# Optimization experiments

Hardware: AMD Instinct MI355X
Metric: run time of the kernel (lower is better)

Reference implementation:

```python
import jax, jax.numpy as jnp
import numpy as np
import math

NUM_BANDS = 16
BINS = 1024
CROPSIZE = 1024
BATCH = 4


def setup_inputs() -> dict:
    key = jax.random.key(0)
    ks = jax.random.split(key, 10)
    s = 1.0 / math.sqrt(BINS)
    return {
        "x": jax.random.normal(ks[0], (BATCH, CROPSIZE, BINS), jnp.float32),
        "Wq": jax.random.normal(ks[1], (BINS, BINS), jnp.float32) * s,
        "bq": jax.random.normal(ks[2], (BINS,), jnp.float32) * 0.02,
        "Wk": jax.random.normal(ks[3], (BINS, BINS), jnp.float32) * s,
        "bk": jax.random.normal(ks[4], (BINS,), jnp.float32) * 0.02,
        "Wv": jax.random.normal(ks[5], (BINS, BINS), jnp.float32) * s,
        "bv": jax.random.normal(ks[6], (BINS,), jnp.float32) * 0.02,
        "Wo": jax.random.normal(ks[7], (BINS, BINS), jnp.float32) * s,
        "bo": jax.random.normal(ks[8], (BINS,), jnp.float32) * 0.02,
        "er": jax.random.normal(ks[9], (BINS // NUM_BANDS, CROPSIZE), jnp.float32),
    }


def reference(x, Wq, bq, Wk, bk, Wv, bv, Wo, bo, er):
    b, w, c = x.shape
    h = NUM_BANDS
    d = c // h
    # Linear projections (torch Linear: x @ W.T + b)
    q = (jnp.einsum("bwc,oc->bwo", x, Wq) + bq).reshape(b, w, h, d).transpose(0, 2, 1, 3)  # [b,h,w,d]
    k = (jnp.einsum("bwc,oc->bwo", x, Wk) + bk).reshape(b, w, h, d).transpose(0, 2, 1, 3)  # [b,h,w,d]
    v = (jnp.einsum("bwc,oc->bwo", x, Wv) + bv).reshape(b, w, h, d).transpose(0, 2, 1, 3)  # [b,h,w,d]
    # relative-position bias via skew trick
    qe = jnp.einsum("bhwd,dc->bhwc", q, er)  # [b,h,w,cropsize]
    qe = jnp.pad(qe, ((0, 0), (0, 0), (0, 0), (1, 0)))  # pad last dim on left -> [b,h,w,crop+1]
    p = jnp.swapaxes(qe, 2, 3)[:, :, 1:, :]  # [b,h,crop,w] == [b,h,w,w] since crop==w
    qk = (jnp.einsum("bhwd,bhud->bhwu", q, k) + p) / math.sqrt(c)
    a = jax.nn.softmax(qk, axis=-1)
    av = jnp.einsum("bhwu,bhud->bhwd", a, v).transpose(0, 2, 1, 3).reshape(b, w, c)
    return jnp.einsum("bwc,oc->bwo", av, Wo) + bo
```

## Files before the change

### kernel.cpp

```cpp
#include <hip/hip_runtime.h>
#include <stdint.h>

typedef __attribute__((ext_vector_type(8))) short   short8;
typedef __attribute__((ext_vector_type(8))) __bf16  bf16x8;
typedef __attribute__((ext_vector_type(4))) float   floatx4;

__device__ __forceinline__ float bf2f(uint16_t h) {
    union { uint32_t u; float f; } v; v.u = ((uint32_t)h) << 16; return v.f;
}
__device__ __forceinline__ uint16_t f2bf(float f) {
    union { float f; uint32_t u; } v; v.f = f;
    uint32_t u = v.u;
    u += 0x7FFFu + ((u >> 16) & 1u);
    return (uint16_t)(u >> 16);
}
__device__ __forceinline__ floatx4 mfma16(short8 a, short8 b, floatx4 c) {
    return __builtin_amdgcn_mfma_f32_16x16x32_bf16(
        __builtin_bit_cast(bf16x8, a), __builtin_bit_cast(bf16x8, b), c, 0, 0, 0);
}
__device__ __forceinline__ void gll16(const short* g, short* l) {
    __builtin_amdgcn_global_load_lds(
        (const __attribute__((address_space(1))) uint32_t*)g,
        (__attribute__((address_space(3))) uint32_t*)l, 16, 0, 0);
}

__global__ void conv_all(
    const float* __restrict__ x,
    const float* __restrict__ Wq, const float* __restrict__ Wk,
    const float* __restrict__ Wv, const float* __restrict__ Wo,
    const float* __restrict__ bq, const float* __restrict__ bk,
    const float* __restrict__ bv, const float* __restrict__ bo,
    const float* __restrict__ er,
    short* __restrict__ xb, short* __restrict__ Wb,
    short* __restrict__ ball, short* __restrict__ ErT)
{
    int blk = blockIdx.x, tid = threadIdx.x;
    if (blk < 4096) {
        int i = blk * 256 + tid;
        float4 v = ((const float4*)x)[i];
        ((short4*)xb)[i] = make_short4((short)f2bf(v.x), (short)f2bf(v.y),
                                       (short)f2bf(v.z), (short)f2bf(v.w));
    } else if (blk < 8192) {
        int rel = blk - 4096;
        int wsel = rel >> 10;
        int i = (rel & 1023) * 256 + tid;
        const float* W = (wsel == 0) ? Wq : (wsel == 1) ? Wk : (wsel == 2) ? Wv : Wo;
        float4 v = ((const float4*)W)[i];
        ((short4*)(Wb + ((size_t)wsel << 20)))[i] =
            make_short4((short)f2bf(v.x), (short)f2bf(v.y),
                        (short)f2bf(v.z), (short)f2bf(v.w));
    } else if (blk < 8448) {
        int idx = (blk - 8192) * 256 + tid;
        int w = idx >> 6, d = idx & 63;
        ErT[idx] = (short)f2bf(er[d * 1024 + w]);
    } else {
        int idx = (blk - 8448) * 256 + tid;
        int sel = idx >> 10, j = idx & 1023;
        const float* s = (sel == 0) ? bq : (sel == 1) ? bk : (sel == 2) ? bv : bo;
        ball[idx] = (short)f2bf(s[j]);
    }
}

#define VM0  asm volatile("s_waitcnt vmcnt(0)" ::: "memory")
#define BARR asm volatile("s_barrier" ::: "memory")

__device__ __forceinline__ void stage_unit(const short* src, short* region, int tid)
{
    const int row  = tid >> 3;
    const int scol = (((tid & 7) ^ (row & 7)) << 3);
    gll16(src + (size_t)row * 1024 + scol, region + tid * 8);
}

#define SAU(buf, u) (As + (buf) * 16384 + (u) * 4096)
#define SBU(buf, u) (Bs + (buf) * 12288 + (u) * 4096)
#define STG_A(buf, u, kt) stage_unit(Asrc + (size_t)(u) * 65536 + (size_t)(kt) * 64, SAU(buf, u), tid)
#define STG_B(buf, u, kt) stage_unit(Bsrc + (size_t)(u) * 65536 + (size_t)(kt) * 64, SBU(buf, u), tid)
#define STG7(buf, kt) do { \
    STG_A(buf, 0, kt); STG_A(buf, 1, kt); STG_A(buf, 2, kt); STG_A(buf, 3, kt); \
    STG_B(buf, 0, kt); STG_B(buf, 1, kt); STG_B(buf, 2, kt); } while (0)

#define RD_A(buf) do { \
    _Pragma("unroll") for (int fr_ = 0; fr_ < 8; ++fr_) { \
        const short* p_ = SAU(buf, wm * 2 + (fr_ >> 2)) + ((fr_ & 3) * 16 + lrow) * 64; \
        _Pragma("unroll") for (int ks_ = 0; ks_ < 2; ++ks_) \
            a[fr_][ks_] = *(const short8*)&p_[((ks_ * 4 + quad) ^ rx) << 3]; \
    } } while (0)

#define RD_B(buf, c) do { \
    const short* p_ = SBU(buf, c) + (wn * 16 + lrow) * 64; \
    _Pragma("unroll") for (int ks_ = 0; ks_ < 2; ++ks_) \
        bb[ks_] = *(const short8*)&p_[((ks_ * 4 + quad) ^ rx) << 3]; \
    } while (0)

#define MFMA_PH(c) do { \
    __builtin_amdgcn_s_setprio(1); \
    _Pragma("unroll") for (int ks_ = 0; ks_ < 2; ++ks_) \
        _Pragma("unroll") for (int fr_ = 0; fr_ < 8; ++fr_) \
            acc[fr_][c] = mfma16(a[fr_][ks_], bb[ks_], acc[fr_][c]); \
    __builtin_amdgcn_s_setprio(0); \
    } while (0)

__global__ __launch_bounds__(512, 2) void qkv_gemm2ph(
    const short* __restrict__ x, const short* __restrict__ Wb,
    const short* __restrict__ ball,
    short* __restrict__ Qb, short* __restrict__ Kb, short* __restrict__ Vb)
{
    extern __shared__ short lds[];
    short* As = lds;
    short* Bs = lds + 32768;
    const int tid  = threadIdx.x;
    const int wid  = tid >> 6;
    const int lane = tid & 63;
    const int wm   = wid >> 2;
    const int wn   = wid & 3;
    const int lrow = lane & 15;
    const int quad = lane >> 4;
    const int rx   = lrow & 7;
    const int bid  = blockIdx.x;
    const int xcd  = bid & 7, gg = bid >> 3;
    const int mi   = (xcd >> 1) * 4 + (gg & 3);
    const int ni   = (xcd & 1) * 8 + (gg >> 2);
    const int m0   = mi * 256, n0 = ni * 192;
    const short* Asrc = x  + (size_t)m0 * 1024;
    const short* Bsrc = Wb + (size_t)n0 * 1024;

    floatx4 acc[8][3];
#pragma unroll
    for (int r = 0; r < 8; ++r)
#pragma unroll
        for (int c = 0; c < 3; ++c) acc[r][c] = (floatx4){0.f, 0.f, 0.f, 0.f};

    short8 a[8][2], bb[2];

    STG7(0, 0);
    VM0; BARR;

#pragma unroll 2
    for (int t = 0; t < 16; ++t) {
        const int cur = t & 1;
        if (t < 15) STG7(cur ^ 1, t + 1);
        RD_A(cur);
        RD_B(cur, 0); MFMA_PH(0);
        RD_B(cur, 1); MFMA_PH(1);
        RD_B(cur, 2); MFMA_PH(2);
        VM0; BARR;
    }

#pragma unroll
    for (int fc = 0; fc < 3; ++fc) {
        int col = n0 + fc * 64 + wn * 16 + lrow;
        int z   = col >> 10;
        int c1  = col & 1023;
        short* dst = (z == 0) ? Qb : (z == 1) ? Kb : Vb;
        float bv = bf2f((uint16_t)ball[col]);
#pragma unroll
        for (int fr = 0; fr < 8; ++fr) {
#pragma unroll
            for (int g = 0; g < 4; ++g) {
                int m = m0 + wm * 128 + fr * 16 + quad * 4 + g;
                float fv = acc[fr][fc][g] + bv;
                int bh = (m >> 10) * 16 + (c1 >> 6);
                if (z == 2)
                    dst[(size_t)bh * 65536 + (size_t)(c1 & 63) * 1024 + (m & 1023)] =
                        (short)f2bf(fv);
                else
                    dst[(size_t)bh * 65536 + (size_t)(m & 1023) * 64 + (c1 & 63)] =
                        (short)f2bf(fv);
            }
        }
    }
}

#define SAU2(buf, u) (As2 + (buf) * 8192 + (u) * 4096)
#define SBU2(buf, u) (Bs2 + (buf) * 8192 + (u) * 4096)
#define STG4(buf, kt) do { \
    stage_unit(Asrc + 0 * 65536 + (size_t)(kt) * 64, SAU2(buf, 0), tid); \
    stage_unit(Asrc + 1 * 65536 + (size_t)(kt) * 64, SAU2(buf, 1), tid); \
    stage_unit(Bsrc + 0 * 65536 + (size_t)(kt) * 64, SBU2(buf, 0), tid); \
    stage_unit(Bsrc + 1 * 65536 + (size_t)(kt) * 64, SBU2(buf, 1), tid); } while (0)

#define RD_A2(buf) do { \
    _Pragma("unroll") for (int fr_ = 0; fr_ < 4; ++fr_) { \
        const short* p_ = SAU2(buf, wm) + (fr_ * 16 + lrow) * 64; \
        _Pragma("unroll") for (int ks_ = 0; ks_ < 2; ++ks_) \
            a[fr_][ks_] = *(const short8*)&p_[((ks_ * 4 + quad) ^ rx) << 3]; \
    } } while (0)

#define RD_B2(buf, c) do { \
    const short* p_ = SBU2(buf, c) + (wn * 16 + lrow) * 64; \
    _Pragma("unroll") for (int ks_ = 0; ks_ < 2; ++ks_) \
        bb[ks_] = *(const short8*)&p_[((ks_ * 4 + quad) ^ rx) << 3]; \
    } while (0)

#define MFMA_PH2(c) do { \
    __builtin_amdgcn_s_setprio(1); \
    _Pragma("unroll") for (int ks_ = 0; ks_ < 2; ++ks_) \
        _Pragma("unroll") for (int fr_ = 0; fr_ < 4; ++fr_) \
            acc[fr_][c] = mfma16(a[fr_][ks_], bb[ks_], acc[fr_][c]); \
    __builtin_amdgcn_s_setprio(0); \
    } while (0)

__global__ __launch_bounds__(512, 2) void out_gemm2ph(
    const short* __restrict__ AV, const short* __restrict__ Wo,
    const short* __restrict__ bo, float* __restrict__ out)
{
    __shared__ short As2[2 * 2 * 4096];
    __shared__ short Bs2[2 * 2 * 4096];
    const int tid  = threadIdx.x;
    const int wid  = tid >> 6;
    const int lane = tid & 63;
    const int wm   = wid >> 2;
    const int wn   = wid & 3;
    const int lrow = lane & 15;
    const int quad = lane >> 4;
    const int rx   = lrow & 7;
    const int bid  = blockIdx.x + blockIdx.y * 32;
    const int xcd  = bid & 7, gg = bid >> 3;
    const int mi   = (xcd & 3) * 8 + (gg & 7);
    const int ni   = (xcd >> 2) * 4 + (gg >> 3);
    const int m0   = mi * 128, n0 = ni * 128;
    const short* Asrc = AV + (size_t)m0 * 1024;
    const short* Bsrc = Wo + (size_t)n0 * 1024;

    floatx4 acc[4][2];
#pragma unroll
    for (int r = 0; r < 4; ++r)
#pragma unroll
        for (int c = 0; c < 2; ++c) acc[r][c] = (floatx4){0.f, 0.f, 0.f, 0.f};

    short8 a[4][2], bb[2];

    STG4(0, 0);
    VM0; BARR;

#pragma unroll 2
    for (int t = 0; t < 16; ++t) {
        const int cur = t & 1;
        if (t < 15) STG4(cur ^ 1, t + 1);
        RD_A2(cur);
        RD_B2(cur, 0); MFMA_PH2(0);
        RD_B2(cur, 1); MFMA_PH2(1);
        VM0; BARR;
    }

#pragma unroll
    for (int fc = 0; fc < 2; ++fc) {
        int col = n0 + fc * 64 + wn * 16 + lrow;
        float bv = bf2f((uint16_t)bo[col]);
#pragma unroll
        for (int fr = 0; fr < 4; ++fr) {
#pragma unroll
            for (int g = 0; g < 4; ++g) {
                int m = m0 + wm * 64 + fr * 16 + quad * 4 + g;
                out[(size_t)m * 1024 + col] = acc[fr][fc][g] + bv;
            }
        }
    }
}

#define PSTR 72
__global__ __launch_bounds__(512, 4) void attn_kernel(
    const short* __restrict__ Q, const short* __restrict__ K,
    const short* __restrict__ Vt, const short* __restrict__ ErT,
    short* __restrict__ AV)
{
    __shared__ short smem[33792];
    short* Ks  = smem;
    short* Qks = smem + 8192;
    short* Vs  = smem + 16384;
    short* Ps  = smem + 24576;
    float* oaccS = (float*)smem;
    float* lrunS = ((float*)smem) + 128 * 65;

    const int tid  = threadIdx.x;
    const int wid  = tid >> 6;
    const int lane = tid & 63;
    const int rg   = wid >> 1;
    const int cg   = wid & 1;
    const int lrow = lane & 15;
    const int quad = lane >> 4;
    const int lk   = quad * 8;
    const int srow = lane >> 3;
    const int sscol = (((lane & 7) ^ (srow & 7)) << 3);
    const int rx = lrow & 7;
    const int h = blockIdx.x, b = blockIdx.y;
    const int bh = b * 16 + h;
    const int i0 = blockIdx.z * 128;
    const short* Qbh = Q  + (size_t)bh * 65536;
    const short* Kbh = K  + (size_t)bh * 65536;
    const short* Vbh = Vt + (size_t)bh * 65536;

    short8 qa[2][4];
#pragma unroll
    for (int m = 0; m < 2; ++m) {
        int row = i0 + rg * 32 + m * 16 + lrow;
#pragma unroll
        for (int kk = 0; kk < 2; ++kk) {
            qa[m][kk]     = *(const short8*)&Qbh[(size_t)row * 64 + kk * 32 + lk];
            qa[m][kk + 2] = *(const short8*)&ErT[(size_t)row * 64 + kk * 32 + lk];
        }
    }

    float lrun[2][4];
    floatx4 oacc[2][4];
#pragma unroll
    for (int m = 0; m < 2; ++m) {
#pragma unroll
        for (int g = 0; g < 4; ++g) lrun[m][g] = 0.f;
#pragma unroll
        for (int c = 0; c < 4; ++c) oacc[m][c] = (floatx4){0.f, 0.f, 0.f, 0.f};
    }

    gll16(Kbh + (size_t)(wid * 8 + srow) * 64 + sscol,    Ks  + wid * 512 + lane * 8);
    gll16(Qbh + (size_t)(wid * 8 + srow) * 64 + sscol,    Qks + wid * 512 + lane * 8);
    gll16(Vbh + (size_t)(wid * 8 + srow) * 1024 + sscol,  Vs  + wid * 512 + lane * 8);

    const float sc2 = 1.44269504088896f / 32.0f;

    for (int jt = 0; jt < 16; ++jt) {
        const int cur = jt & 1;
        __syncthreads();

        if (jt < 15) {
            int j1 = (jt + 1) * 64;
            gll16(Kbh + (size_t)(j1 + wid * 8 + srow) * 64 + sscol,    Ks  + (cur ^ 1) * 4096 + wid * 512 + lane * 8);
            gll16(Qbh + (size_t)(j1 + wid * 8 + srow) * 64 + sscol,    Qks + (cur ^ 1) * 4096 + wid * 512 + lane * 8);
            gll16(Vbh + (size_t)(wid * 8 + srow) * 1024 + j1 + sscol,  Vs  + (cur ^ 1) * 4096 + wid * 512 + lane * 8);
        }

        floatx4 s[2][2];
#pragma unroll
        for (int m = 0; m < 2; ++m)
#pragma unroll
            for (int c = 0; c < 2; ++c) s[m][c] = (floatx4){0.f, 0.f, 0.f, 0.f};
#pragma unroll
        for (int kk = 0; kk < 4; ++kk) {
            short8 kb[2];
            const short* src = ((kk < 2) ? Ks : Qks) + cur * 4096;
            const int kl = kk & 1;
#pragma unroll
            for (int c = 0; c < 2; ++c)
                kb[c] = *(const short8*)&src[(cg * 32 + c * 16 + lrow) * 64 +
                                             (((kl * 4 + quad) ^ rx) << 3)];
#pragma unroll
            for (int m = 0; m < 2; ++m)
#pragma unroll
                for (int c = 0; c < 2; ++c)
                    s[m][c] = mfma16(qa[m][kk], kb[c], s[m][c]);
        }

#pragma unroll
        for (int m = 0; m < 2; ++m)
#pragma unroll
            for (int c = 0; c < 2; ++c)
#pragma unroll
                for (int g = 0; g < 4; ++g)
                    s[m][c][g] = exp2f(s[m][c][g] * sc2);
#pragma unroll
        for (int m = 0; m < 2; ++m)
#pragma unroll
            for (int g = 0; g < 4; ++g)
                lrun[m][g] += s[m][0][g] + s[m][1][g];

#pragma unroll
        for (int m = 0; m < 2; ++m)
#pragma unroll
            for (int c = 0; c < 2; ++c)
#pragma unroll
                for (int g = 0; g < 4; ++g)
                    Ps[(rg * 32 + m * 16 + quad * 4 + g) * PSTR + cg * 32 + c * 16 + lrow] =
                        (short)f2bf(s[m][c][g]);
        __asm__ __volatile__("" ::: "memory");

        {
            short8 pa[2], vb[4];
#pragma unroll
            for (int m = 0; m < 2; ++m)
                pa[m] = *(const short8*)&Ps[(rg * 32 + m * 16 + lrow) * PSTR + cg * 32 + lk];
#pragma unroll
            for (int c = 0; c < 4; ++c)
                vb[c] = *(const short8*)&Vs[cur * 4096 + (c * 16 + lrow) * 64 +
                                            (((cg * 4 + quad) ^ rx) << 3)];
#pragma unroll
            for (int m = 0; m < 2; ++m)
#pragma unroll
                for (int c = 0; c < 4; ++c)
                    oacc[m][c] = mfma16(pa[m], vb[c], oacc[m][c]);
        }
    }

#pragma unroll
    for (int m = 0; m < 2; ++m)
#pragma unroll
        for (int g = 0; g < 4; ++g) {
            float r = lrun[m][g];
#pragma unroll
            for (int d = 1; d < 16; d <<= 1) r += __shfl_xor(r, d, 64);
            lrun[m][g] = r;
        }

    __syncthreads();
    if (cg == 0) {
#pragma unroll
        for (int m = 0; m < 2; ++m) {
#pragma unroll
            for (int c = 0; c < 4; ++c)
#pragma unroll
                for (int g = 0; g < 4; ++g)
                    oaccS[(rg * 32 + m * 16 + quad * 4 + g) * 65 + c * 16 + lrow] =
                        oacc[m][c][g];
            if (lrow == 0)
#pragma unroll
                for (int g = 0; g < 4; ++g)
                    lrunS[rg * 32 + m * 16 + quad * 4 + g] = lrun[m][g];
        }
    }
    __syncthreads();
    if (cg == 1) {
#pragma unroll
        for (int m = 0; m < 2; ++m)
#pragma unroll
            for (int g = 0; g < 4; ++g) {
                int row = rg * 32 + m * 16 + quad * 4 + g;
                float lt = lrun[m][g] + lrunS[row];
#pragma unroll
                for (int c = 0; c < 4; ++c) {
                    float tot = oacc[m][c][g] + oaccS[row * 65 + c * 16 + lrow];
                    AV[((size_t)b * 1024 + i0 + row) * 1024 + h * 64 + c * 16 + lrow] =
                        (short)f2bf(tot / lt);
                }
            }
    }
}

extern "C" void kernel_launch(void* const* d_in, const int* in_sizes, int n_in,
                              void* d_out, int out_size, void* d_ws, size_t ws_size,
                              hipStream_t stream) {
    const float* x  = (const float*)d_in[0];
    const float* Wq = (const float*)d_in[1];
    const float* bq = (const float*)d_in[2];
    const float* Wk = (const float*)d_in[3];
    const float* bk = (const float*)d_in[4];
    const float* Wv = (const float*)d_in[5];
    const float* bv = (const float*)d_in[6];
    const float* Wo = (const float*)d_in[7];
    const float* bo = (const float*)d_in[8];
    const float* er = (const float*)d_in[9];
    float* out = (float*)d_out;

    const size_t M1 = 1u << 20;
    short* ws   = (short*)d_ws;
    short* xb   = (short*)d_out;
    short* Qb   = ws;
    short* Kb   = ws + 4 * M1;
    short* Vb   = ws + 8 * M1;
    short* AVb  = ws + 12 * M1;
    short* Wb   = ws + 16 * M1;
    short* ball = ws + 20 * M1;
    short* ErT  = ws + 20 * M1 + 4096;

    static bool attr_done = false;
    if (!attr_done) {
        hipFuncSetAttribute((const void*)qkv_gemm2ph,
                            hipFuncAttributeMaxDynamicSharedMemorySize, 114688);
        attr_done = true;
    }

    hipLaunchKernelGGL(conv_all, dim3(8464), dim3(256), 0, stream,
                       x, Wq, Wk, Wv, Wo, bq, bk, bv, bo, er, xb, Wb, ball, ErT);
    hipLaunchKernelGGL(qkv_gemm2ph, dim3(256), dim3(512), 114688, stream,
                       xb, Wb, ball, Qb, Kb, Vb);
    hipLaunchKernelGGL(attn_kernel, dim3(16, 4, 8), dim3(512), 0, stream,
                       Qb, Kb, Vb, ErT, AVb);
    hipLaunchKernelGGL(out_gemm2ph, dim3(32, 8), dim3(512), 0, stream,
                       AVb, Wb + 3 * M1, ball + 3072, out);
}
```

Measured before the change: 196.9 us.

## Halve attention query tile and read skew-bias Q from global instead of LDS

The attention kernel now processes 64 query rows per block instead of 128, doubling the grid to 1024 blocks and raising the launch-bounds occupancy hint. The Q tile used for the relative-position skew term is no longer staged in LDS; each wave loads it directly from global memory, which shrinks shared memory per block. The aim is more resident blocks and better latency hiding. The cost is that K and V tiles are reloaded twice as often overall, and the Q reads are unpipelined global loads on the critical path.

```diff
diff --git a/kernel.cpp b/kernel.cpp
--- a/kernel.cpp
+++ b/kernel.cpp
@@ -259,18 +259,17 @@
 }
 
 #define PSTR 72
-__global__ __launch_bounds__(512, 4) void attn_kernel(
+__global__ __launch_bounds__(512, 6) void attn_kernel(
     const short* __restrict__ Q, const short* __restrict__ K,
     const short* __restrict__ Vt, const short* __restrict__ ErT,
     short* __restrict__ AV)
 {
-    __shared__ short smem[33792];
+    __shared__ short smem[20992];
     short* Ks  = smem;
-    short* Qks = smem + 8192;
-    short* Vs  = smem + 16384;
-    short* Ps  = smem + 24576;
+    short* Vs  = smem + 8192;
+    short* Ps  = smem + 16384;
     float* oaccS = (float*)smem;
-    float* lrunS = ((float*)smem) + 128 * 65;
+    float* lrunS = ((float*)smem) + 64 * 65;
 
     const int tid  = threadIdx.x;
     const int wid  = tid >> 6;
@@ -285,35 +284,30 @@
     const int rx = lrow & 7;
     const int h = blockIdx.x, b = blockIdx.y;
     const int bh = b * 16 + h;
-    const int i0 = blockIdx.z * 128;
+    const int i0 = blockIdx.z * 64;
     const short* Qbh = Q  + (size_t)bh * 65536;
     const short* Kbh = K  + (size_t)bh * 65536;
     const short* Vbh = Vt + (size_t)bh * 65536;
 
-    short8 qa[2][4];
-#pragma unroll
-    for (int m = 0; m < 2; ++m) {
-        int row = i0 + rg * 32 + m * 16 + lrow;
+    short8 qa[4];
+    {
+        int row = i0 + rg * 16 + lrow;
 #pragma unroll
         for (int kk = 0; kk < 2; ++kk) {
-            qa[m][kk]     = *(const short8*)&Qbh[(size_t)row * 64 + kk * 32 + lk];
-            qa[m][kk + 2] = *(const short8*)&ErT[(size_t)row * 64 + kk * 32 + lk];
-        }
-    }
-
-    float lrun[2][4];
-    floatx4 oacc[2][4];
-#pragma unroll
-    for (int m = 0; m < 2; ++m) {
-#pragma unroll
-        for (int g = 0; g < 4; ++g) lrun[m][g] = 0.f;
-#pragma unroll
-        for (int c = 0; c < 4; ++c) oacc[m][c] = (floatx4){0.f, 0.f, 0.f, 0.f};
-    }
-
-    gll16(Kbh + (size_t)(wid * 8 + srow) * 64 + sscol,    Ks  + wid * 512 + lane * 8);
-    gll16(Qbh + (size_t)(wid * 8 + srow) * 64 + sscol,    Qks + wid * 512 + lane * 8);
-    gll16(Vbh + (size_t)(wid * 8 + srow) * 1024 + sscol,  Vs  + wid * 512 + lane * 8);
+            qa[kk]     = *(const short8*)&Qbh[(size_t)row * 64 + kk * 32 + lk];
+            qa[kk + 2] = *(const short8*)&ErT[(size_t)row * 64 + kk * 32 + lk];
+        }
+    }
+
+    float lrun[4];
+    floatx4 oacc[4];
+#pragma unroll
+    for (int g = 0; g < 4; ++g) lrun[g] = 0.f;
+#pragma unroll
+    for (int c = 0; c < 4; ++c) oacc[c] = (floatx4){0.f, 0.f, 0.f, 0.f};
+
+    gll16(Kbh + (size_t)(wid * 8 + srow) * 64 + sscol,    Ks + wid * 512 + lane * 8);
+    gll16(Vbh + (size_t)(wid * 8 + srow) * 1024 + sscol,  Vs + wid * 512 + lane * 8);
 
     const float sc2 = 1.44269504088896f / 32.0f;
 
@@ -323,113 +317,102 @@
 
         if (jt < 15) {
             int j1 = (jt + 1) * 64;
-            gll16(Kbh + (size_t)(j1 + wid * 8 + srow) * 64 + sscol,    Ks  + (cur ^ 1) * 4096 + wid * 512 + lane * 8);
-            gll16(Qbh + (size_t)(j1 + wid * 8 + srow) * 64 + sscol,    Qks + (cur ^ 1) * 4096 + wid * 512 + lane * 8);
-            gll16(Vbh + (size_t)(wid * 8 + srow) * 1024 + j1 + sscol,  Vs  + (cur ^ 1) * 4096 + wid * 512 + lane * 8);
-        }
-
-        floatx4 s[2][2];
-#pragma unroll
-        for (int m = 0; m < 2; ++m)
-#pragma unroll
-            for (int c = 0; c < 2; ++c) s[m][c] = (floatx4){0.f, 0.f, 0.f, 0.f};
-#pragma unroll
-        for (int kk = 0; kk < 4; ++kk) {
+            gll16(Kbh + (size_t)(j1 + wid * 8 + srow) * 64 + sscol,    Ks + (cur ^ 1) * 4096 + wid * 512 + lane * 8);
+            gll16(Vbh + (size_t)(wid * 8 + srow) * 1024 + j1 + sscol,  Vs + (cur ^ 1) * 4096 + wid * 512 + lane * 8);
+        }
+
+        short8 qj[2][2];
+#pragma unroll
+        for (int kl = 0; kl < 2; ++kl)
+#pragma unroll
+            for (int c = 0; c < 2; ++c)
+                qj[kl][c] = *(const short8*)&Qbh[
+                    (size_t)(jt * 64 + cg * 32 + c * 16 + lrow) * 64 + kl * 32 + lk];
+
+        floatx4 s[2];
+#pragma unroll
+        for (int c = 0; c < 2; ++c) s[c] = (floatx4){0.f, 0.f, 0.f, 0.f};
+#pragma unroll
+        for (int kk = 0; kk < 2; ++kk) {
             short8 kb[2];
-            const short* src = ((kk < 2) ? Ks : Qks) + cur * 4096;
-            const int kl = kk & 1;
 #pragma unroll
             for (int c = 0; c < 2; ++c)
-                kb[c] = *(const short8*)&src[(cg * 32 + c * 16 + lrow) * 64 +
-                                             (((kl * 4 + quad) ^ rx) << 3)];
-#pragma unroll
-            for (int m = 0; m < 2; ++m)
-#pragma unroll
-                for (int c = 0; c < 2; ++c)
-                    s[m][c] = mfma16(qa[m][kk], kb[c], s[m][c]);
-        }
-
-#pragma unroll
-        for (int m = 0; m < 2; ++m)
+                kb[c] = *(const short8*)&Ks[cur * 4096 +
+                                            (cg * 32 + c * 16 + lrow) * 64 +
+                                            (((kk * 4 + quad) ^ rx) << 3)];
 #pragma unroll
             for (int c = 0; c < 2; ++c)
-#pragma unroll
-                for (int g = 0; g < 4; ++g)
-                    s[m][c][g] = exp2f(s[m][c][g] * sc2);
-#pragma unroll
-        for (int m = 0; m < 2; ++m)
+                s[c] = mfma16(qa[kk], kb[c], s[c]);
+        }
+#pragma unroll
+        for (int kl = 0; kl < 2; ++kl)
+#pragma unroll
+            for (int c = 0; c < 2; ++c)
+                s[c] = mfma16(qa[kl + 2], qj[kl][c], s[c]);
+
+#pragma unroll
+        for (int c = 0; c < 2; ++c)
 #pragma unroll
             for (int g = 0; g < 4; ++g)
-                lrun[m][g] += s[m][0][g] + s[m][1][g];
-
-#pragma unroll
-        for (int m = 0; m < 2; ++m)
-#pragma unroll
-            for (int c = 0; c < 2; ++c)
-#pragma unroll
-                for (int g = 0; g < 4; ++g)
-                    Ps[(rg * 32 + m * 16 + quad * 4 + g) * PSTR + cg * 32 + c * 16 + lrow] =
-                        (short)f2bf(s[m][c][g]);
+                s[c][g] = exp2f(s[c][g] * sc2);
+#pragma unroll
+        for (int g = 0; g < 4; ++g)
+            lrun[g] += s[0][g] + s[1][g];
+
+#pragma unroll
+        for (int c = 0; c < 2; ++c)
+#pragma unroll
+            for (int g = 0; g < 4; ++g)
+                Ps[(rg * 16 + quad * 4 + g) * PSTR + cg * 32 + c * 16 + lrow] =
+                    (short)f2bf(s[c][g]);
         __asm__ __volatile__("" ::: "memory");
 
         {
-            short8 pa[2], vb[4];
-#pragma unroll
-            for (int m = 0; m < 2; ++m)
-                pa[m] = *(const short8*)&Ps[(rg * 32 + m * 16 + lrow) * PSTR + cg * 32 + lk];
+            short8 pa, vb[4];
+            pa = *(const short8*)&Ps[(rg * 16 + lrow) * PSTR + cg * 32 + lk];
 #pragma unroll
             for (int c = 0; c < 4; ++c)
                 vb[c] = *(const short8*)&Vs[cur * 4096 + (c * 16 + lrow) * 64 +
                                             (((cg * 4 + quad) ^ rx) << 3)];
 #pragma unroll
-            for (int m = 0; m < 2; ++m)
-#pragma unroll
-                for (int c = 0; c < 4; ++c)
-                    oacc[m][c] = mfma16(pa[m], vb[c], oacc[m][c]);
-        }
-    }
-
-#pragma unroll
-    for (int m = 0; m < 2; ++m)
-#pragma unroll
-        for (int g = 0; g < 4; ++g) {
-            float r = lrun[m][g];
-#pragma unroll
-            for (int d = 1; d < 16; d <<= 1) r += __shfl_xor(r, d, 64);
-            lrun[m][g] = r;
-        }
+            for (int c = 0; c < 4; ++c)
+                oacc[c] = mfma16(pa, vb[c], oacc[c]);
+        }
+    }
+
+#pragma unroll
+    for (int g = 0; g < 4; ++g) {
+        float r = lrun[g];
+#pragma unroll
+        for (int d = 1; d < 16; d <<= 1) r += __shfl_xor(r, d, 64);
+        lrun[g] = r;
+    }
 
     __syncthreads();
     if (cg == 0) {
 #pragma unroll
-        for (int m = 0; m < 2; ++m) {
-#pragma unroll
-            for (int c = 0; c < 4; ++c)
-#pragma unroll
-                for (int g = 0; g < 4; ++g)
-                    oaccS[(rg * 32 + m * 16 + quad * 4 + g) * 65 + c * 16 + lrow] =
-                        oacc[m][c][g];
-            if (lrow == 0)
-#pragma unroll
-                for (int g = 0; g < 4; ++g)
-                    lrunS[rg * 32 + m * 16 + quad * 4 + g] = lrun[m][g];
-        }
+        for (int c = 0; c < 4; ++c)
+#pragma unroll
+            for (int g = 0; g < 4; ++g)
+                oaccS[(rg * 16 + quad * 4 + g) * 65 + c * 16 + lrow] = oacc[c][g];
+        if (lrow == 0)
+#pragma unroll
+            for (int g = 0; g < 4; ++g)
+                lrunS[rg * 16 + quad * 4 + g] = lrun[g];
     }
     __syncthreads();
     if (cg == 1) {
 #pragma unroll
-        for (int m = 0; m < 2; ++m)
-#pragma unroll
-            for (int g = 0; g < 4; ++g) {
-                int row = rg * 32 + m * 16 + quad * 4 + g;
-                float lt = lrun[m][g] + lrunS[row];
-#pragma unroll
-                for (int c = 0; c < 4; ++c) {
-                    float tot = oacc[m][c][g] + oaccS[row * 65 + c * 16 + lrow];
-                    AV[((size_t)b * 1024 + i0 + row) * 1024 + h * 64 + c * 16 + lrow] =
-                        (short)f2bf(tot / lt);
-                }
+        for (int g = 0; g < 4; ++g) {
+            int row = rg * 16 + quad * 4 + g;
+            float lt = lrun[g] + lrunS[row];
+#pragma unroll
+            for (int c = 0; c < 4; ++c) {
+                float tot = oacc[c][g] + oaccS[row * 65 + c * 16 + lrow];
+                AV[((size_t)b * 1024 + i0 + row) * 1024 + h * 64 + c * 16 + lrow] =
+                    (short)f2bf(tot / lt);
             }
+        }
     }
 }
 
@@ -470,7 +453,7 @@
                        x, Wq, Wk, Wv, Wo, bq, bk, bv, bo, er, xb, Wb, ball, ErT);
     hipLaunchKernelGGL(qkv_gemm2ph, dim3(256), dim3(512), 114688, stream,
                        xb, Wb, ball, Qb, Kb, Vb);
-    hipLaunchKernelGGL(attn_kernel, dim3(16, 4, 8), dim3(512), 0, stream,
+    hipLaunchKernelGGL(attn_kernel, dim3(16, 4, 16), dim3(512), 0, stream,
                        Qb, Kb, Vb, ErT, AVb);
     hipLaunchKernelGGL(out_gemm2ph, dim3(32, 8), dim3(512), 0, stream,
                        AVb, Wb + 3 * M1, ball + 3072, out);
```

New measurement: 235.3 us. 19.5% more time.
